# Optimization experiments

Hardware: AMD Instinct MI355X
Metric: run time of the kernel (lower is better)

The kernel has to match this reference:

```python
import jax, jax.numpy as jnp
import numpy as np

D_MODEL = 1024
NUM_HEADS = 16
HEAD_DIM = D_MODEL // NUM_HEADS
ROPE_BASE = 10000.0


def _rope_cos_sin(seq_len, head_dim, dtype):
    # inv_freq over half the head dim (standard 1D RoPE)
    inv_freq = 1.0 / (ROPE_BASE ** (jnp.arange(0, head_dim, 2, dtype=jnp.float32) / head_dim))
    ang = jnp.arange(seq_len, dtype=jnp.float32)[:, None] * inv_freq[None, :]  # [S, hd/2]
    cos = jnp.concatenate([jnp.cos(ang), jnp.cos(ang)], axis=-1).astype(dtype)  # [S, hd]
    sin = jnp.concatenate([jnp.sin(ang), jnp.sin(ang)], axis=-1).astype(dtype)
    return cos, sin


def _rotate_half(t):
    t1, t2 = jnp.split(t, 2, axis=-1)
    return jnp.concatenate([-t2, t1], axis=-1)


def _apply_rope(t, cos, sin):
    # t: [B, H, S, hd]; cos/sin: [S, hd]
    return t * cos[None, None, :, :] + _rotate_half(t) * sin[None, None, :, :]


def setup_inputs() -> dict:
    key = jax.random.key(0)
    k1, k2, k3 = jax.random.split(key, 3)
    B, S = 2, 2048
    x = jax.random.normal(k1, (B, S, D_MODEL), dtype=jnp.float32)
    w_qkv = jax.random.normal(k2, (D_MODEL, 3 * D_MODEL), dtype=jnp.float32) * (D_MODEL ** -0.5)
    w_proj = jax.random.normal(k3, (D_MODEL, D_MODEL), dtype=jnp.float32) * (D_MODEL ** -0.5)
    b_proj = jnp.zeros((D_MODEL,), dtype=jnp.float32)
    return {"x": x, "w_qkv": w_qkv, "w_proj": w_proj, "b_proj": b_proj, "causal": 1}


def reference(x, w_qkv, w_proj, b_proj, causal):
    B, S, D = x.shape
    scale = HEAD_DIM ** -0.5
    qkv = x @ w_qkv  # [B, S, 3D]
    q, k, v = jnp.split(qkv, 3, axis=-1)

    def to_heads(t):
        return t.reshape(B, S, NUM_HEADS, HEAD_DIM).transpose(0, 2, 1, 3)  # [B,H,S,hd]

    q, k, v = to_heads(q), to_heads(k), to_heads(v)

    cos, sin = _rope_cos_sin(S, HEAD_DIM, x.dtype)
    q = _apply_rope(q, cos, sin)
    k = _apply_rope(k, cos, sin)

    attn = jnp.einsum('bhqd,bhkd->bhqk', q, k) * scale  # [B,H,S,S]
    if causal:
        causal_mask = jnp.triu(jnp.ones((S, S), dtype=bool), k=1)
        attn = jnp.where(causal_mask[None, None, :, :], jnp.float32(-jnp.inf).astype(attn.dtype), attn)
    attn = jax.nn.softmax(attn, axis=-1)
    out = jnp.einsum('bhqk,bhkd->bhqd', attn, v)  # [B,H,S,hd]
    out = out.transpose(0, 2, 1, 3).reshape(B, S, D)
    return out @ w_proj + b_proj
```

## Files before the change

kernel.cpp:

```cpp
#include <hip/hip_runtime.h>
#include <stdint.h>
#include <math.h>

#define B_   2
#define S_   2048
#define D_   1024
#define H_   16
#define HD_  64
#define M_   (B_*S_)
#define N3_  (3*D_)

typedef __bf16 bf16;
typedef __bf16 bf16x2 __attribute__((ext_vector_type(2)));
typedef __bf16 bf16x4v __attribute__((ext_vector_type(4)));
typedef __bf16 bf16x8 __attribute__((ext_vector_type(8)));
typedef float  f32x4 __attribute__((ext_vector_type(4)));
typedef float  f32x16 __attribute__((ext_vector_type(16)));

__device__ __forceinline__ void gload_lds16(const void* g, void* l) {
  __builtin_amdgcn_global_load_lds(
      (__attribute__((address_space(1))) const unsigned int*)g,
      (__attribute__((address_space(3))) unsigned int*)l, 16, 0, 0);
}

__global__ __launch_bounds__(256) void prep_kernel(const float* __restrict__ x, bf16* __restrict__ xb,
                                                   const float* __restrict__ w_qkv, bf16* __restrict__ wqkvT,
                                                   const float* __restrict__ w_proj, bf16* __restrict__ wprojT,
                                                   float* __restrict__ cosT, float* __restrict__ sinT) {
  __shared__ float tile[32][33];
  int blk = blockIdx.x, tid = threadIdx.x;
  if (blk < 1024) {
#pragma unroll
    for (int it = 0; it < 4; it++) {
      int i = (blk * 4 + it) * 256 + tid;
      float4 v = ((const float4*)x)[i];
      bf16x4v o;
      o[0] = (bf16)v.x; o[1] = (bf16)v.y; o[2] = (bf16)v.z; o[3] = (bf16)v.w;
      *(bf16x4v*)(xb + (size_t)i * 4) = o;
    }
  } else if (blk < 5120) {
    const float* in; bf16* out; int R, C, tb;
    if (blk < 4096) { in = w_qkv;  out = wqkvT;  R = 1024; C = 3072; tb = blk - 1024; }
    else            { in = w_proj; out = wprojT; R = 1024; C = 1024; tb = blk - 4096; }
    int nbx = C >> 5;
    int bx = tb % nbx, by = tb / nbx;
    int c0 = bx * 32, r0 = by * 32;
    int tx = tid & 31, ty = tid >> 5;
#pragma unroll
    for (int j = 0; j < 4; j++)
      tile[ty + j * 8][tx] = in[(size_t)(r0 + ty + j * 8) * C + c0 + tx];
    __syncthreads();
#pragma unroll
    for (int j = 0; j < 4; j++)
      out[(size_t)(c0 + ty + j * 8) * R + r0 + tx] = (bf16)tile[tx][ty + j * 8];
  } else {
    int i = (blk - 5120) * 256 + tid;
    int s = i >> 5, d = i & 31;
    float inv = powf(10000.0f, -(float)d * (1.0f / 32.0f));
    float a = (float)s * inv;
    float sv, cv;
    sincosf(a, &sv, &cv);
    cosT[i] = cv; sinT[i] = sv;
  }
}

__global__ __launch_bounds__(256) void gemm128(const bf16* __restrict__ A,
                                               const bf16* __restrict__ Bt,
                                               int M, int N, int K,
                                               bf16* __restrict__ Cb,
                                               const float* __restrict__ cosT,
                                               const float* __restrict__ sinT,
                                               bf16* __restrict__ vt) {
  __shared__ bf16 As[128 * 32];
  __shared__ bf16 Bs[128 * 32];
  int tid = threadIdx.x;
  int lane = tid & 63, w = tid >> 6;
  int nwg = gridDim.x * gridDim.y;
  int bid = blockIdx.y * gridDim.x + blockIdx.x;
  int sw = (bid & 7) * (nwg >> 3) + (bid >> 3);
  int bx = sw % gridDim.x, by = sw / gridDim.x;
  int m0 = by * 128, n0 = bx * 128;
  int m_off = (w >> 1) * 64, n_off = (w & 1) * 64;
  f32x4 acc[4][4] = {};

  const char* Ab = (const char*)A;
  const char* Bb = (const char*)Bt;
  int srow = (lane >> 2);
  int skb  = (lane & 3) * 16;

  for (int k0 = 0; k0 < K; k0 += 32) {
    for (int j = 0; j < 2; j++) {
      int seg = j * 4 + w;
      int row = seg * 16 + srow;
      gload_lds16(Ab + ((size_t)(m0 + row) * K + k0) * 2 + skb, (char*)As + seg * 1024);
      gload_lds16(Bb + ((size_t)(n0 + row) * K + k0) * 2 + skb, (char*)Bs + seg * 1024);
    }
    __syncthreads();
    int rl = lane & 15;
    int kgb = (lane >> 4) * 16;
    bf16x8 a[4], b[4];
    for (int i = 0; i < 4; i++)
      a[i] = *(const bf16x8*)((const char*)As + (m_off + i * 16 + rl) * 64 + kgb);
    for (int i = 0; i < 4; i++)
      b[i] = *(const bf16x8*)((const char*)Bs + (n_off + i * 16 + rl) * 64 + kgb);
    for (int i = 0; i < 4; i++)
      for (int j = 0; j < 4; j++)
        acc[i][j] = __builtin_amdgcn_mfma_f32_16x16x32_bf16(a[i], b[j], acc[i][j], 0, 0, 0);
    __syncthreads();
  }

  int rq = (lane >> 4) * 4, cl = lane & 15;
  if ((n0 + n_off) < 2048) {
    for (int i = 0; i < 4; i++)
      for (int r = 0; r < 4; r++) {
        int row = m0 + m_off + i * 16 + rq + r;
        int srw = row & 2047;
        for (int j = 0; j < 2; j++) {
          int d2 = j * 16 + cl;
          float c = cosT[srw * 32 + d2], sn = sinT[srw * 32 + d2];
          float x1 = acc[i][j][r], x2 = acc[i][j + 2][r];
          Cb[(size_t)row * N + n0 + n_off + d2]      = (bf16)(x1 * c - x2 * sn);
          Cb[(size_t)row * N + n0 + n_off + d2 + 32] = (bf16)(x2 * c + x1 * sn);
        }
      }
  } else {
    int posbase = ((rq & 4) << 1) | ((rq & 8) >> 1);
    for (int i = 0; i < 4; i++) {
      int row0 = m0 + m_off + i * 16;
      int b = row0 >> 11;
      int sbase = (row0 & 2047) + posbase;
      for (int j = 0; j < 4; j++) {
        int col = n0 + n_off + j * 16 + cl - 2048;
        bf16x4v pv;
        pv[0] = (bf16)acc[i][j][0]; pv[1] = (bf16)acc[i][j][1];
        pv[2] = (bf16)acc[i][j][2]; pv[3] = (bf16)acc[i][j][3];
        *(bf16x4v*)(vt + ((size_t)(b * 1024 + col)) * 2048 + sbase) = pv;
      }
    }
  }
}

__global__ __launch_bounds__(256) void gemm_proj(const bf16* __restrict__ A,
                                                 const bf16* __restrict__ Bt,
                                                 float* __restrict__ Cf,
                                                 const float* __restrict__ bias) {
  __shared__ bf16 As[64 * 32];
  __shared__ bf16 Bs[128 * 32];
  const int K = 1024, N = 1024;
  int tid = threadIdx.x;
  int lane = tid & 63, w = tid >> 6;
  int bid = blockIdx.y * gridDim.x + blockIdx.x;
  int sw = (bid & 7) * 64 + (bid >> 3);
  int bx = sw & 7, by = sw >> 3;
  int m0 = by * 64, n0 = bx * 128;
  int m_off = (w >> 1) * 32, n_off = (w & 1) * 64;
  f32x4 acc[2][4] = {};

  const char* Ab = (const char*)A;
  const char* Bb = (const char*)Bt;
  int arow = tid >> 2, achk = (tid & 3) * 16;

  for (int k0 = 0; k0 < K; k0 += 32) {
    gload_lds16(Ab + ((size_t)(m0 + arow) * K + k0) * 2 + achk, (char*)As + tid * 16);
    gload_lds16(Bb + ((size_t)(n0 + arow) * K + k0) * 2 + achk, (char*)Bs + tid * 16);
    gload_lds16(Bb + ((size_t)(n0 + 64 + arow) * K + k0) * 2 + achk, (char*)Bs + 4096 + tid * 16);
    __syncthreads();
    int rl = lane & 15;
    int kgb = (lane >> 4) * 16;
    bf16x8 a[2], b[4];
    for (int i = 0; i < 2; i++)
      a[i] = *(const bf16x8*)((const char*)As + (m_off + i * 16 + rl) * 64 + kgb);
    for (int j = 0; j < 4; j++)
      b[j] = *(const bf16x8*)((const char*)Bs + (n_off + j * 16 + rl) * 64 + kgb);
    for (int i = 0; i < 2; i++)
      for (int j = 0; j < 4; j++)
        acc[i][j] = __builtin_amdgcn_mfma_f32_16x16x32_bf16(a[i], b[j], acc[i][j], 0, 0, 0);
    __syncthreads();
  }

  int rq = (lane >> 4) * 4, cl = lane & 15;
  for (int i = 0; i < 2; i++)
    for (int j = 0; j < 4; j++) {
      int col = n0 + n_off + j * 16 + cl;
      float bv = bias[col];
      for (int r = 0; r < 4; r++) {
        int row = m0 + m_off + i * 16 + rq + r;
        Cf[(size_t)row * N + col] = acc[i][j][r] + bv;
      }
    }
}

__global__ __launch_bounds__(512, 4) void attn_kernel(const bf16* __restrict__ qkv,
                                                      const bf16* __restrict__ vt,
                                                      bf16* __restrict__ O) {
  __shared__ __align__(16) unsigned char Ks[2][16384];
  __shared__ __align__(16) unsigned char Vs[2][16384];
  int tid = threadIdx.x, lane = tid & 63, w = tid >> 6;
  int qw = w & 3, p = w >> 2;
  int bid = blockIdx.x;
  int xcd = bid & 7, slot = bid >> 3;
  int bh = xcd * 4 + (slot & 3);
  int u = slot >> 2;
  int qt = 15 - u;
  int b = bh >> 4, h = bh & 15;
  int q0w = qt * 128 + qw * 32;
  int l31 = lane & 31, hi = lane >> 5;
  const char* qb = (const char*)qkv;
  const char* vb = (const char*)vt;

  int kr0 = tid >> 3, kcs = (tid & 7) ^ (kr0 & 7);
  int vr0 = tid >> 4, vcs = (tid & 15) ^ (vr0 & 7);

#define STAGE(buf, kvbase)                                                                              \
  do {                                                                                                  \
    gload_lds16(qb + (((size_t)(b * 2048 + (kvbase) + kr0) * 3072) + 1024 + h * 64) * 2 + kcs * 16,     \
                (char*)Ks[buf] + tid * 16);                                                             \
    gload_lds16(qb + (((size_t)(b * 2048 + (kvbase) + kr0 + 64) * 3072) + 1024 + h * 64) * 2 + kcs * 16,\
                (char*)Ks[buf] + (tid + 512) * 16);                                                     \
    gload_lds16(vb + (((size_t)(bh * 64 + vr0) * 2048) + (kvbase)) * 2 + vcs * 16,                      \
                (char*)Vs[buf] + tid * 16);                                                             \
    gload_lds16(vb + (((size_t)(bh * 64 + vr0 + 32) * 2048) + (kvbase)) * 2 + vcs * 16,                 \
                (char*)Vs[buf] + (tid + 512) * 16);                                                     \
  } while (0)

  bf16x8 aq[4];
#pragma unroll
  for (int s = 0; s < 4; s++) {
    size_t row = (size_t)(b * 2048 + q0w + l31);
    bf16x8 v = *(const bf16x8*)(qb + (row * 3072 + h * 64 + s * 16 + hi * 8) * 2);
#pragma unroll
    for (int e = 0; e < 8; e++) v[e] = (bf16)((float)v[e] * 0.18033688f);
    aq[s] = v;
  }

  f32x16 o0 = {}, o1 = {};
  float mrun = -3e38f, lrun = 0.f;
  int npair = qt + 1;

  STAGE(0, 0);
  asm volatile("s_waitcnt vmcnt(0)" ::: "memory");
  __builtin_amdgcn_s_barrier();

  for (int i = 0; i < npair; i++) {
    int cur = i & 1;
    if (i + 1 < npair) STAGE(cur ^ 1, (i + 1) * 128);

    int kvw = i * 128 + p * 64;
    if (kvw <= q0w + 31) {
      bool diag = (kvw + 63 > q0w);

      f32x16 scr[2];
#pragma unroll
      for (int kf = 0; kf < 2; kf++)
#pragma unroll
        for (int r = 0; r < 16; r++) scr[kf][r] = 0.f;
      __builtin_amdgcn_s_setprio(1);
#pragma unroll
      for (int s = 0; s < 4; s++) {
#pragma unroll
        for (int kf = 0; kf < 2; kf++) {
          int row = p * 64 + kf * 32 + l31;
          int ch = (hi + 2 * s) ^ (row & 7);
          bf16x8 ak = *(const bf16x8*)(Ks[cur] + row * 128 + ch * 16);
          scr[kf] = __builtin_amdgcn_mfma_f32_32x32x16_bf16(ak, aq[s], scr[kf], 0, 0, 0);
        }
      }
      __builtin_amdgcn_s_setprio(0);

      int qg = q0w + l31;
      if (diag) {
#pragma unroll
        for (int kf = 0; kf < 2; kf++)
#pragma unroll
          for (int r = 0; r < 16; r++) {
            int k = kvw + kf * 32 + (r & 3) + 8 * (r >> 2) + 4 * hi;
            if (k > qg) scr[kf][r] = -3e38f;
          }
      }

      float mx = -3e38f;
#pragma unroll
      for (int kf = 0; kf < 2; kf++)
#pragma unroll
        for (int r = 0; r < 16; r++) mx = fmaxf(mx, scr[kf][r]);
      mx = fmaxf(mx, __shfl_xor(mx, 32));

      if (!__all(mx - mrun <= 11.5f)) {
        float mnew = fmaxf(mrun, mx);
        float corr = exp2f(mrun - mnew);
        mrun = mnew;
        lrun *= corr;
#pragma unroll
        for (int r = 0; r < 16; r++) {
          float cr = __shfl(corr, (r & 3) + 8 * (r >> 2) + 4 * hi);
          o0[r] *= cr; o1[r] *= cr;
        }
      }

      float rs = 0.f;
      unsigned D[2][8];
#pragma unroll
      for (int kf = 0; kf < 2; kf++)
#pragma unroll
        for (int j = 0; j < 8; j++) {
          float p0 = exp2f(scr[kf][2 * j] - mrun);
          float p1 = exp2f(scr[kf][2 * j + 1] - mrun);
          rs += p0 + p1;
          bf16x2 tp; tp[0] = (bf16)p0; tp[1] = (bf16)p1;
          D[kf][j] = __builtin_bit_cast(unsigned, tp);
        }
      rs += __shfl_xor(rs, 32);
      lrun += rs;

#pragma unroll
      for (int kf = 0; kf < 2; kf++) {
#pragma unroll
        for (int sg = 0; sg < 2; sg++) {
          union { unsigned u4[4]; bf16x8 v; } ap;
          ap.u4[0] = D[kf][4 * sg + 0];
          ap.u4[1] = D[kf][4 * sg + 1];
          ap.u4[2] = D[kf][4 * sg + 2];
          ap.u4[3] = D[kf][4 * sg + 3];
          __builtin_amdgcn_s_setprio(1);
#pragma unroll
          for (int nf = 0; nf < 2; nf++) {
            int row = nf * 32 + l31;
            int ch = ((p * 8) + (hi + 2 * sg + 4 * kf)) ^ (row & 7);
            bf16x8 bv = *(const bf16x8*)(Vs[cur] + row * 256 + ch * 16);
            if (nf == 0) o0 = __builtin_amdgcn_mfma_f32_32x32x16_bf16(ap.v, bv, o0, 0, 0, 0);
            else         o1 = __builtin_amdgcn_mfma_f32_32x32x16_bf16(ap.v, bv, o1, 0, 0, 0);
          }
          __builtin_amdgcn_s_setprio(0);
        }
      }
    }

    asm volatile("s_waitcnt vmcnt(0)" ::: "memory");
    __builtin_amdgcn_s_barrier();
  }

  float* mlb = (float*)Ks;
  if (hi == 0) {
    mlb[((qw * 2 + p) * 2 + 0) * 32 + l31] = mrun;
    mlb[((qw * 2 + p) * 2 + 1) * 32 + l31] = lrun;
  }
  __syncthreads();
  float m_o = mlb[((qw * 2 + (1 - p)) * 2 + 0) * 32 + l31];
  float l_o = mlb[((qw * 2 + (1 - p)) * 2 + 1) * 32 + l31];
  float Mm = fmaxf(mrun, m_o);
  float cs = exp2f(mrun - Mm);
  float L  = lrun * cs + l_o * exp2f(m_o - Mm);
  float* obuf = (float*)Vs;
  if (p == 1) {
#pragma unroll
    for (int r = 0; r < 16; r++) {
      int crow = (r & 3) + 8 * (r >> 2) + 4 * hi;
      float c = __shfl(cs, crow);
      obuf[qw * 2048 + r * 64 + lane]        = o0[r] * c;
      obuf[qw * 2048 + (r + 16) * 64 + lane] = o1[r] * c;
    }
  }
  __syncthreads();
  if (p == 0) {
    float linv = 1.0f / L;
#pragma unroll
    for (int r = 0; r < 16; r++) {
      int crow = (r & 3) + 8 * (r >> 2) + 4 * hi;
      float c  = __shfl(cs, crow);
      float li = __shfl(linv, crow);
      size_t row = (size_t)(b * 2048 + q0w + crow);
      float v0 = (o0[r] * c + obuf[qw * 2048 + r * 64 + lane]) * li;
      float v1 = (o1[r] * c + obuf[qw * 2048 + (r + 16) * 64 + lane]) * li;
      O[row * 1024 + h * 64 + l31]      = (bf16)v0;
      O[row * 1024 + h * 64 + 32 + l31] = (bf16)v1;
    }
  }
#undef STAGE
}

extern "C" void kernel_launch(void* const* d_in, const int* in_sizes, int n_in,
                              void* d_out, int out_size, void* d_ws, size_t ws_size,
                              hipStream_t stream) {
  const float* x      = (const float*)d_in[0];
  const float* w_qkv  = (const float*)d_in[1];
  const float* w_proj = (const float*)d_in[2];
  const float* b_proj = (const float*)d_in[3];

  char* ws = (char*)d_ws;
  size_t off = 0;
  bf16* xb     = (bf16*)(ws + off); off += (size_t)M_ * D_ * 2;
  bf16* wqkvT  = (bf16*)(ws + off); off += (size_t)N3_ * D_ * 2;
  bf16* wprojT = (bf16*)(ws + off); off += (size_t)D_ * D_ * 2;
  bf16* qkvb   = (bf16*)(ws + off); off += (size_t)M_ * N3_ * 2;
  bf16* ob     = (bf16*)(ws + off); off += (size_t)M_ * D_ * 2;
  bf16* vtb    = (bf16*)(ws + off); off += (size_t)M_ * D_ * 2;
  float* cosT  = (float*)(ws + off); off += (size_t)S_ * 32 * 4;
  float* sinT  = (float*)(ws + off); off += (size_t)S_ * 32 * 4;

  prep_kernel<<<5376, 256, 0, stream>>>(x, xb, w_qkv, wqkvT, w_proj, wprojT, cosT, sinT);
  gemm128<<<dim3(N3_ / 128, M_ / 128), 256, 0, stream>>>(xb, wqkvT, M_, N3_, D_, qkvb, cosT, sinT, vtb);
  attn_kernel<<<512, 512, 0, stream>>>(qkvb, vtb, ob);
  gemm_proj<<<dim3(8, 64), 256, 0, stream>>>(ob, wprojT, (float*)d_out, b_proj);
}
```

Measured before the change: 113.5 us.

## Rewrite QKV GEMM with 256x256 tiles and double-buffered swizzled LDS pipeline

Replaces the 128x128 QKV GEMM with a 512-thread 256x256 tile kernel that uses 128KB of double-buffered LDS with XOR-swizzled layout and issues global-to-LDS loads interleaved with MFMA phases under explicit barriers and priority hints. This aims to hide global load latency and cut the per-k-step synchronisation of the old single-buffered loop. The larger tile yields only 192 blocks, which may leave compute units idle, and the heavy LDS use limits occupancy to one block per CU.

New measurement: 110.4 us. -2.7%, faster.

```diff
diff --git a/kernel.cpp b/kernel.cpp
--- a/kernel.cpp
+++ b/kernel.cpp
@@ -64,80 +64,226 @@
   }
 }
 
-__global__ __launch_bounds__(256) void gemm128(const bf16* __restrict__ A,
-                                               const bf16* __restrict__ Bt,
-                                               int M, int N, int K,
-                                               bf16* __restrict__ Cb,
-                                               const float* __restrict__ cosT,
-                                               const float* __restrict__ sinT,
-                                               bf16* __restrict__ vt) {
-  __shared__ bf16 As[128 * 32];
-  __shared__ bf16 Bs[128 * 32];
-  int tid = threadIdx.x;
-  int lane = tid & 63, w = tid >> 6;
-  int nwg = gridDim.x * gridDim.y;
+__global__ __launch_bounds__(512, 2) void gemm_qkv(const bf16* __restrict__ A,
+                                                   const bf16* __restrict__ Bt,
+                                                   bf16* __restrict__ Cb,
+                                                   const float* __restrict__ cosT,
+                                                   const float* __restrict__ sinT,
+                                                   bf16* __restrict__ vt) {
+  __shared__ __align__(16) unsigned char lds[131072];
+  const int K = 1024;
+  int tid = threadIdx.x, lane = tid & 63, w = tid >> 6;
+  int wm = w >> 2, wn = w & 3;
   int bid = blockIdx.y * gridDim.x + blockIdx.x;
-  int sw = (bid & 7) * (nwg >> 3) + (bid >> 3);
-  int bx = sw % gridDim.x, by = sw / gridDim.x;
-  int m0 = by * 128, n0 = bx * 128;
-  int m_off = (w >> 1) * 64, n_off = (w & 1) * 64;
-  f32x4 acc[4][4] = {};
-
-  const char* Ab = (const char*)A;
-  const char* Bb = (const char*)Bt;
-  int srow = (lane >> 2);
-  int skb  = (lane & 3) * 16;
-
-  for (int k0 = 0; k0 < K; k0 += 32) {
-    for (int j = 0; j < 2; j++) {
-      int seg = j * 4 + w;
-      int row = seg * 16 + srow;
-      gload_lds16(Ab + ((size_t)(m0 + row) * K + k0) * 2 + skb, (char*)As + seg * 1024);
-      gload_lds16(Bb + ((size_t)(n0 + row) * K + k0) * 2 + skb, (char*)Bs + seg * 1024);
-    }
-    __syncthreads();
-    int rl = lane & 15;
-    int kgb = (lane >> 4) * 16;
-    bf16x8 a[4], b[4];
-    for (int i = 0; i < 4; i++)
-      a[i] = *(const bf16x8*)((const char*)As + (m_off + i * 16 + rl) * 64 + kgb);
-    for (int i = 0; i < 4; i++)
-      b[i] = *(const bf16x8*)((const char*)Bs + (n_off + i * 16 + rl) * 64 + kgb);
-    for (int i = 0; i < 4; i++)
-      for (int j = 0; j < 4; j++)
-        acc[i][j] = __builtin_amdgcn_mfma_f32_16x16x32_bf16(a[i], b[j], acc[i][j], 0, 0, 0);
-    __syncthreads();
-  }
-
-  int rq = (lane >> 4) * 4, cl = lane & 15;
-  if ((n0 + n_off) < 2048) {
-    for (int i = 0; i < 4; i++)
+  int sw = (bid & 7) * 24 + (bid >> 3);
+  int bx = sw % 12, by = sw / 12;
+  int m0 = by * 256, n0 = bx * 256;
+  int rl = lane & 15, kg = lane >> 4;
+
+  int l3 = lane >> 3;
+  int cS = ((lane & 7) ^ l3) * 16;
+  const char* sA = (const char*)A  + ((size_t)(m0 + w * 32 + l3) * K) * 2 + cS;
+  const char* sB = (const char*)Bt + ((size_t)(n0 + w * 32 + l3) * K) * 2 + cS;
+  char* dA = (char*)lds + w * 4096 + lane * 16;
+  char* dB = dA + 32768;
+
+#define STG(kt, s)                                                                   \
+  do {                                                                               \
+    const int _j = (s) & 3;                                                          \
+    const int _bo = ((kt) & 1) << 16;                                                \
+    if ((s) < 4) gload_lds16(sA + (size_t)_j * 16384 + (size_t)(kt) * 128,           \
+                             dA + _bo + _j * 1024);                                  \
+    else         gload_lds16(sB + (size_t)_j * 16384 + (size_t)(kt) * 128,           \
+                             dB + _bo + _j * 1024);                                  \
+  } while (0)
+
+  int chunkv[2];
+  chunkv[0] = ((0 + kg) ^ (rl & 7)) * 16;
+  chunkv[1] = ((4 + kg) ^ (rl & 7)) * 16;
+  int base_a = (wm * 128 + rl) * 128;
+  int base_b = 32768 + (wn * 64 + rl) * 128;
+
+#define RDA(Lb, ar, ks) (*(const bf16x8*)((Lb) + base_a + (ar) * 2048 + chunkv[ks]))
+#define RDB(Lb, br, ks) (*(const bf16x8*)((Lb) + base_b + (br) * 2048 + chunkv[ks]))
+#define BARR() asm volatile("s_barrier" ::: "memory")
+#define VM2()  asm volatile("s_waitcnt vmcnt(2)" ::: "memory")
+
+  f32x4 acc[8][4] = {};
+  bf16x8 a[4][2], b[4][2];
+
+#pragma unroll
+  for (int s = 0; s < 8; s++) { STG(0, s); STG(1, s); }
+  asm volatile("s_waitcnt vmcnt(0)" ::: "memory");
+  BARR();
+
+  for (int i = 0; i < 8; i++) {
+    int t0 = 2 * i, t1 = t0 + 1;
+    const char* L0 = (const char*)lds;
+    const char* L1 = (const char*)lds + 65536;
+
+    VM2();
+#pragma unroll
+    for (int ar = 0; ar < 4; ar++) { a[ar][0] = RDA(L0, ar, 0); a[ar][1] = RDA(L0, ar, 1); }
+#pragma unroll
+    for (int br = 0; br < 2; br++) { b[br][0] = RDB(L0, br, 0); b[br][1] = RDB(L0, br, 1); }
+    if (i) { STG(t1, 2); STG(t1, 3); }
+    BARR();
+    __builtin_amdgcn_s_setprio(1);
+#pragma unroll
+    for (int ar = 0; ar < 4; ar++)
+#pragma unroll
+      for (int br = 0; br < 2; br++) {
+        acc[ar][br] = __builtin_amdgcn_mfma_f32_16x16x32_bf16(a[ar][0], b[br][0], acc[ar][br], 0, 0, 0);
+        acc[ar][br] = __builtin_amdgcn_mfma_f32_16x16x32_bf16(a[ar][1], b[br][1], acc[ar][br], 0, 0, 0);
+      }
+    __builtin_amdgcn_s_setprio(0);
+    BARR();
+
+#pragma unroll
+    for (int br = 2; br < 4; br++) { b[br][0] = RDB(L0, br, 0); b[br][1] = RDB(L0, br, 1); }
+    if (i) { STG(t1, 4); STG(t1, 5); }
+    BARR();
+    __builtin_amdgcn_s_setprio(1);
+#pragma unroll
+    for (int ar = 0; ar < 4; ar++)
+#pragma unroll
+      for (int br = 2; br < 4; br++) {
+        acc[ar][br] = __builtin_amdgcn_mfma_f32_16x16x32_bf16(a[ar][0], b[br][0], acc[ar][br], 0, 0, 0);
+        acc[ar][br] = __builtin_amdgcn_mfma_f32_16x16x32_bf16(a[ar][1], b[br][1], acc[ar][br], 0, 0, 0);
+      }
+    __builtin_amdgcn_s_setprio(0);
+    BARR();
+
+#pragma unroll
+    for (int ar = 0; ar < 4; ar++) { a[ar][0] = RDA(L0, ar + 4, 0); a[ar][1] = RDA(L0, ar + 4, 1); }
+    if (i) { STG(t1, 6); STG(t1, 7); }
+    BARR();
+    __builtin_amdgcn_s_setprio(1);
+#pragma unroll
+    for (int ar = 0; ar < 4; ar++)
+#pragma unroll
+      for (int br = 0; br < 2; br++) {
+        acc[ar + 4][br] = __builtin_amdgcn_mfma_f32_16x16x32_bf16(a[ar][0], b[br][0], acc[ar + 4][br], 0, 0, 0);
+        acc[ar + 4][br] = __builtin_amdgcn_mfma_f32_16x16x32_bf16(a[ar][1], b[br][1], acc[ar + 4][br], 0, 0, 0);
+      }
+    __builtin_amdgcn_s_setprio(0);
+    BARR();
+
+    if (t0 + 2 < 16) { STG(t0 + 2, 0); STG(t0 + 2, 1); }
+    BARR();
+    __builtin_amdgcn_s_setprio(1);
+#pragma unroll
+    for (int ar = 0; ar < 4; ar++)
+#pragma unroll
+      for (int br = 2; br < 4; br++) {
+        acc[ar + 4][br] = __builtin_amdgcn_mfma_f32_16x16x32_bf16(a[ar][0], b[br][0], acc[ar + 4][br], 0, 0, 0);
+        acc[ar + 4][br] = __builtin_amdgcn_mfma_f32_16x16x32_bf16(a[ar][1], b[br][1], acc[ar + 4][br], 0, 0, 0);
+      }
+    __builtin_amdgcn_s_setprio(0);
+    BARR();
+
+    VM2();
+#pragma unroll
+    for (int ar = 0; ar < 4; ar++) { a[ar][0] = RDA(L1, ar, 0); a[ar][1] = RDA(L1, ar, 1); }
+#pragma unroll
+    for (int br = 0; br < 2; br++) { b[br][0] = RDB(L1, br, 0); b[br][1] = RDB(L1, br, 1); }
+    if (t0 + 2 < 16) { STG(t0 + 2, 2); STG(t0 + 2, 3); }
+    BARR();
+    __builtin_amdgcn_s_setprio(1);
+#pragma unroll
+    for (int ar = 0; ar < 4; ar++)
+#pragma unroll
+      for (int br = 0; br < 2; br++) {
+        acc[ar][br] = __builtin_amdgcn_mfma_f32_16x16x32_bf16(a[ar][0], b[br][0], acc[ar][br], 0, 0, 0);
+        acc[ar][br] = __builtin_amdgcn_mfma_f32_16x16x32_bf16(a[ar][1], b[br][1], acc[ar][br], 0, 0, 0);
+      }
+    __builtin_amdgcn_s_setprio(0);
+    BARR();
+
+#pragma unroll
+    for (int br = 2; br < 4; br++) { b[br][0] = RDB(L1, br, 0); b[br][1] = RDB(L1, br, 1); }
+    if (t0 + 2 < 16) { STG(t0 + 2, 4); STG(t0 + 2, 5); }
+    BARR();
+    __builtin_amdgcn_s_setprio(1);
+#pragma unroll
+    for (int ar = 0; ar < 4; ar++)
+#pragma unroll
+      for (int br = 2; br < 4; br++) {
+        acc[ar][br] = __builtin_amdgcn_mfma_f32_16x16x32_bf16(a[ar][0], b[br][0], acc[ar][br], 0, 0, 0);
+        acc[ar][br] = __builtin_amdgcn_mfma_f32_16x16x32_bf16(a[ar][1], b[br][1], acc[ar][br], 0, 0, 0);
+      }
+    __builtin_amdgcn_s_setprio(0);
+    BARR();
+
+#pragma unroll
+    for (int ar = 0; ar < 4; ar++) { a[ar][0] = RDA(L1, ar + 4, 0); a[ar][1] = RDA(L1, ar + 4, 1); }
+    if (t0 + 2 < 16) { STG(t0 + 2, 6); STG(t0 + 2, 7); }
+    BARR();
+    __builtin_amdgcn_s_setprio(1);
+#pragma unroll
+    for (int ar = 0; ar < 4; ar++)
+#pragma unroll
+      for (int br = 0; br < 2; br++) {
+        acc[ar + 4][br] = __builtin_amdgcn_mfma_f32_16x16x32_bf16(a[ar][0], b[br][0], acc[ar + 4][br], 0, 0, 0);
+        acc[ar + 4][br] = __builtin_amdgcn_mfma_f32_16x16x32_bf16(a[ar][1], b[br][1], acc[ar + 4][br], 0, 0, 0);
+      }
+    __builtin_amdgcn_s_setprio(0);
+    BARR();
+
+    if (t1 + 2 < 16) { STG(t1 + 2, 0); STG(t1 + 2, 1); }
+    BARR();
+    __builtin_amdgcn_s_setprio(1);
+#pragma unroll
+    for (int ar = 0; ar < 4; ar++)
+#pragma unroll
+      for (int br = 2; br < 4; br++) {
+        acc[ar + 4][br] = __builtin_amdgcn_mfma_f32_16x16x32_bf16(a[ar][0], b[br][0], acc[ar + 4][br], 0, 0, 0);
+        acc[ar + 4][br] = __builtin_amdgcn_mfma_f32_16x16x32_bf16(a[ar][1], b[br][1], acc[ar + 4][br], 0, 0, 0);
+      }
+    __builtin_amdgcn_s_setprio(0);
+    BARR();
+  }
+
+  int rq = kg * 4;
+  if (n0 < 2048) {
+#pragma unroll
+    for (int ar = 0; ar < 8; ar++)
+#pragma unroll
       for (int r = 0; r < 4; r++) {
-        int row = m0 + m_off + i * 16 + rq + r;
+        int row = m0 + wm * 128 + ar * 16 + rq + r;
         int srw = row & 2047;
-        for (int j = 0; j < 2; j++) {
-          int d2 = j * 16 + cl;
+#pragma unroll
+        for (int br = 0; br < 2; br++) {
+          int d2 = br * 16 + rl;
           float c = cosT[srw * 32 + d2], sn = sinT[srw * 32 + d2];
-          float x1 = acc[i][j][r], x2 = acc[i][j + 2][r];
-          Cb[(size_t)row * N + n0 + n_off + d2]      = (bf16)(x1 * c - x2 * sn);
-          Cb[(size_t)row * N + n0 + n_off + d2 + 32] = (bf16)(x2 * c + x1 * sn);
+          float x1 = acc[ar][br][r], x2 = acc[ar][br + 2][r];
+          size_t o = (size_t)row * 3072 + n0 + wn * 64 + d2;
+          Cb[o]      = (bf16)(x1 * c - x2 * sn);
+          Cb[o + 32] = (bf16)(x2 * c + x1 * sn);
         }
       }
   } else {
     int posbase = ((rq & 4) << 1) | ((rq & 8) >> 1);
-    for (int i = 0; i < 4; i++) {
-      int row0 = m0 + m_off + i * 16;
-      int b = row0 >> 11;
+#pragma unroll
+    for (int ar = 0; ar < 8; ar++) {
+      int row0 = m0 + wm * 128 + ar * 16;
+      int bb = row0 >> 11;
       int sbase = (row0 & 2047) + posbase;
-      for (int j = 0; j < 4; j++) {
-        int col = n0 + n_off + j * 16 + cl - 2048;
+#pragma unroll
+      for (int br = 0; br < 4; br++) {
+        int col = n0 + wn * 64 + br * 16 + rl - 2048;
         bf16x4v pv;
-        pv[0] = (bf16)acc[i][j][0]; pv[1] = (bf16)acc[i][j][1];
-        pv[2] = (bf16)acc[i][j][2]; pv[3] = (bf16)acc[i][j][3];
-        *(bf16x4v*)(vt + ((size_t)(b * 1024 + col)) * 2048 + sbase) = pv;
+        pv[0] = (bf16)acc[ar][br][0]; pv[1] = (bf16)acc[ar][br][1];
+        pv[2] = (bf16)acc[ar][br][2]; pv[3] = (bf16)acc[ar][br][3];
+        *(bf16x4v*)(vt + ((size_t)(bb * 1024 + col)) * 2048 + sbase) = pv;
       }
     }
   }
+#undef STG
+#undef RDA
+#undef RDB
+#undef BARR
+#undef VM2
 }
 
 __global__ __launch_bounds__(256) void gemm_proj(const bf16* __restrict__ A,
@@ -398,7 +544,7 @@
   float* sinT  = (float*)(ws + off); off += (size_t)S_ * 32 * 4;
 
   prep_kernel<<<5376, 256, 0, stream>>>(x, xb, w_qkv, wqkvT, w_proj, wprojT, cosT, sinT);
-  gemm128<<<dim3(N3_ / 128, M_ / 128), 256, 0, stream>>>(xb, wqkvT, M_, N3_, D_, qkvb, cosT, sinT, vtb);
+  gemm_qkv<<<dim3(12, 16), 512, 0, stream>>>(xb, wqkvT, qkvb, cosT, sinT, vtb);
   attn_kernel<<<512, 512, 0, stream>>>(qkvb, vtb, ob);
   gemm_proj<<<dim3(8, 64), 256, 0, stream>>>(ob, wprojT, (float*)d_out, b_proj);
 }
```
